# Kernel tuning notes

Measured on AMD Instinct MI355X. Metric: run time of the kernel, lower is better.

## Reference

```python
import jax, jax.numpy as jnp
import numpy as np

LEVEL = 3  # init kwarg: level=3, wavelet_type='db1' (Haar)


def _haar_step(x):
    """One db1/Haar 2x2 stride-2 decomposition on [B,C,H,W].
    conv2d with kernels outer(l,l),outer(l,h),outer(h,l),outer(h,h), l=h=1/sqrt(2),
    reduces to block sum/difference arithmetic with factor 0.5.
    Returns [B, 4*C, H/2, W/2] in the torch code's channel-major layout
    (c0_LL, c0_LH, c0_HL, c0_HH, c1_LL, ...).
    """
    a = x[..., 0::2, 0::2]
    b = x[..., 0::2, 1::2]
    c = x[..., 1::2, 0::2]
    d = x[..., 1::2, 1::2]
    ll = (a + b + c + d) * 0.5
    lh = (a - b + c - d) * 0.5  # low rows x high cols (cross-correlation)
    hl = (a + b - c - d) * 0.5
    hh = (a - b - c + d) * 0.5
    w = jnp.stack([ll, lh, hl, hh], axis=2)  # [B, C, 4, H/2, W/2]
    B, C = x.shape[0], x.shape[1]
    return w.reshape(B, 4 * C, w.shape[3], w.shape[4])


def setup_inputs() -> dict:
    key = jax.random.key(0)
    x = jax.random.normal(key, (4, 32, 512, 512), dtype=jnp.float32)
    return {"x": x}


def reference(x):
    C = x.shape[1]
    current = x
    highs = []
    for _ in range(LEVEL):
        cur4 = _haar_step(current)        # [B, 4C, h, w]
        low = cur4[:, :C]                 # first C of interleaved subband channels (as in torch code)
        highs.append(cur4[:, C:])         # remaining 3C channels
        current = low
    # torch returns (low, [h1, h2, h3, low])
    return (low, highs[0], highs[1], highs[2], low)
```

## Files before the change

kernel.cpp:

```cpp
#include <hip/hip_runtime.h>


__global__ __launch_bounds__(256) void haar_step_kernel(
    const float* __restrict__ in,
    float* __restrict__ low,
    float* __restrict__ high,
    float* __restrict__ low_dup,
    int C, int H, int W, int total)
{
    int tid = blockIdx.x * blockDim.x + threadIdx.x;
    if (tid >= total) return;

    const int OH  = H >> 1;
    const int OW  = W >> 1;
    const int OW2 = OW >> 1;

    int ow2 = tid % OW2;
    int t1  = tid / OW2;
    int oh  = t1 % OH;
    int t2  = t1 / OH;
    int c   = t2 % C;
    int b   = t2 / C;

    const float* rowbase = in + (((size_t)(b * C + c) * H + 2 * oh) * W) + 4 * ow2;
    float4 r0 = *reinterpret_cast<const float4*>(rowbase);
    float4 r1 = *reinterpret_cast<const float4*>(rowbase + W);

    float2 ll, lh, hl, hh;
    ll.x = (r0.x + r0.y + r1.x + r1.y) * 0.5f;
    lh.x = (r0.x - r0.y + r1.x - r1.y) * 0.5f;
    hl.x = (r0.x + r0.y - r1.x - r1.y) * 0.5f;
    hh.x = (r0.x - r0.y - r1.x + r1.y) * 0.5f;
    ll.y = (r0.z + r0.w + r1.z + r1.w) * 0.5f;
    lh.y = (r0.z - r0.w + r1.z - r1.w) * 0.5f;
    hl.y = (r0.z + r0.w - r1.z - r1.w) * 0.5f;
    hh.y = (r0.z - r0.w - r1.z + r1.w) * 0.5f;

    const int    baseoc = 4 * c;
    const size_t cs     = (size_t)OH * OW;
    const size_t sp     = (size_t)oh * OW + 2 * ow2;

    if (baseoc < C) {
        float* p = low + ((size_t)b * C + baseoc) * cs + sp;
        *reinterpret_cast<float2*>(p)          = ll;
        *reinterpret_cast<float2*>(p + cs)     = lh;
        *reinterpret_cast<float2*>(p + 2 * cs) = hl;
        *reinterpret_cast<float2*>(p + 3 * cs) = hh;
        if (low_dup) {
            float* q = low_dup + ((size_t)b * C + baseoc) * cs + sp;
            *reinterpret_cast<float2*>(q)          = ll;
            *reinterpret_cast<float2*>(q + cs)     = lh;
            *reinterpret_cast<float2*>(q + 2 * cs) = hl;
            *reinterpret_cast<float2*>(q + 3 * cs) = hh;
        }
    } else {
        float* p = high + ((size_t)b * (3 * C) + (baseoc - C)) * cs + sp;
        *reinterpret_cast<float2*>(p)          = ll;
        *reinterpret_cast<float2*>(p + cs)     = lh;
        *reinterpret_cast<float2*>(p + 2 * cs) = hl;
        *reinterpret_cast<float2*>(p + 3 * cs) = hh;
    }
}

extern "C" void kernel_launch(void* const* d_in, const int* in_sizes, int n_in,
                              void* d_out, int out_size, void* d_ws, size_t ws_size,
                              hipStream_t stream) {
    const float* x = (const float*)d_in[0];
    float* out = (float*)d_out;

    const int B = 4, C = 32;

    const size_t n_low3  = (size_t)B * C * 64 * 64;
    const size_t n_high1 = (size_t)B * 3 * C * 256 * 256;
    const size_t n_high2 = (size_t)B * 3 * C * 128 * 128;
    const size_t n_high3 = (size_t)B * 3 * C * 64 * 64;

    float* low3_a = out;
    float* high1  = out + n_low3;
    float* high2  = high1 + n_high1;
    float* high3  = high2 + n_high2;
    float* low3_b = high3 + n_high3;

    float* ws1 = (float*)d_ws;
    float* ws2 = ws1 + (size_t)B * C * 256 * 256;

    const int threads = 256;

    {
        int total = B * C * 256 * 128;
        int blocks = (total + threads - 1) / threads;
        haar_step_kernel<<<blocks, threads, 0, stream>>>(
            x, ws1, high1, nullptr, C, 512, 512, total);
    }
    {
        int total = B * C * 128 * 64;
        int blocks = (total + threads - 1) / threads;
        haar_step_kernel<<<blocks, threads, 0, stream>>>(
            ws1, ws2, high2, nullptr, C, 256, 256, total);
    }
    {
        int total = B * C * 64 * 32;
        int blocks = (total + threads - 1) / threads;
        haar_step_kernel<<<blocks, threads, 0, stream>>>(
            ws2, low3_a, high3, low3_b, C, 128, 128, total);
    }
}
```

Before: 246.2 us.

## Fuse three Haar decomposition levels into one register-resident kernel

Replaces three separate Haar-step launches with a single kernel. Each thread loads an 8x8 input patch and computes all three levels in registers, writing each high band directly to its output location. This removes the workspace round trips for the intermediate low bands and two kernel launches. In exchange, register pressure rises, the level-3 stores are scalar and strided across channels, and channels with c>=8 exit early, which leaves work unevenly spread across blocks.

```diff
diff --git a/kernel.cpp b/kernel.cpp
--- a/kernel.cpp
+++ b/kernel.cpp
@@ -1,64 +1,105 @@
 #include <hip/hip_runtime.h>
 
 
-__global__ __launch_bounds__(256) void haar_step_kernel(
-    const float* __restrict__ in,
-    float* __restrict__ low,
-    float* __restrict__ high,
-    float* __restrict__ low_dup,
-    int C, int H, int W, int total)
+#define HAAR(a, b_, c_, d, o0, o1, o2, o3)       \
+    o0 = (a + b_ + c_ + d) * 0.5f;               \
+    o1 = (a - b_ + c_ - d) * 0.5f;               \
+    o2 = (a + b_ - c_ - d) * 0.5f;               \
+    o3 = (a - b_ - c_ + d) * 0.5f;
+
+__global__ __launch_bounds__(256) void haar3_fused(
+    const float* __restrict__ x,
+    float* __restrict__ high1,
+    float* __restrict__ high2,
+    float* __restrict__ high3,
+    float* __restrict__ low3a,
+    float* __restrict__ low3b)
 {
-    int tid = blockIdx.x * blockDim.x + threadIdx.x;
-    if (tid >= total) return;
+    const int tid   = threadIdx.x;
+    const int tx    = tid & 63;
+    const int ty    = tid >> 6;
+    const int tileY = blockIdx.x;
+    const int bc    = blockIdx.y;
+    const int c     = bc & 31;
+    const int b     = bc >> 5;
 
-    const int OH  = H >> 1;
-    const int OW  = W >> 1;
-    const int OW2 = OW >> 1;
+    float w1[4][4][4];
+    {
+        const float* base = x + ((size_t)bc * 512 + (size_t)(tileY * 32 + ty * 8)) * 512
+                              + (size_t)tx * 8;
+        #pragma unroll
+        for (int i = 0; i < 4; ++i) {
+            float4 r0a = *(const float4*)(base + (size_t)(2 * i) * 512);
+            float4 r0b = *(const float4*)(base + (size_t)(2 * i) * 512 + 4);
+            float4 r1a = *(const float4*)(base + (size_t)(2 * i + 1) * 512);
+            float4 r1b = *(const float4*)(base + (size_t)(2 * i + 1) * 512 + 4);
+            HAAR(r0a.x, r0a.y, r1a.x, r1a.y, w1[0][i][0], w1[1][i][0], w1[2][i][0], w1[3][i][0]);
+            HAAR(r0a.z, r0a.w, r1a.z, r1a.w, w1[0][i][1], w1[1][i][1], w1[2][i][1], w1[3][i][1]);
+            HAAR(r0b.x, r0b.y, r1b.x, r1b.y, w1[0][i][2], w1[1][i][2], w1[2][i][2], w1[3][i][2]);
+            HAAR(r0b.z, r0b.w, r1b.z, r1b.w, w1[0][i][3], w1[1][i][3], w1[2][i][3], w1[3][i][3]);
+        }
+    }
 
-    int ow2 = tid % OW2;
-    int t1  = tid / OW2;
-    int oh  = t1 % OH;
-    int t2  = t1 / OH;
-    int c   = t2 % C;
-    int b   = t2 / C;
+    if (c >= 8) {
+        float* hp = high1 + ((size_t)b * 96 + (size_t)(4 * (c - 8))) * (256 * 256)
+                          + (size_t)(tileY * 16 + ty * 4) * 256 + (size_t)tx * 4;
+        #pragma unroll
+        for (int s = 0; s < 4; ++s)
+            #pragma unroll
+            for (int i = 0; i < 4; ++i)
+                *(float4*)(hp + (size_t)s * (256 * 256) + i * 256) =
+                    make_float4(w1[s][i][0], w1[s][i][1], w1[s][i][2], w1[s][i][3]);
+        return;
+    }
 
-    const float* rowbase = in + (((size_t)(b * C + c) * H + 2 * oh) * W) + 4 * ow2;
-    float4 r0 = *reinterpret_cast<const float4*>(rowbase);
-    float4 r1 = *reinterpret_cast<const float4*>(rowbase + W);
+    float w2[16][2][2];
+    #pragma unroll
+    for (int s = 0; s < 4; ++s)
+        #pragma unroll
+        for (int i = 0; i < 2; ++i)
+            #pragma unroll
+            for (int j = 0; j < 2; ++j) {
+                float a  = w1[s][2 * i][2 * j];
+                float bb = w1[s][2 * i][2 * j + 1];
+                float cc = w1[s][2 * i + 1][2 * j];
+                float dd = w1[s][2 * i + 1][2 * j + 1];
+                HAAR(a, bb, cc, dd, w2[4 * s + 0][i][j], w2[4 * s + 1][i][j],
+                                    w2[4 * s + 2][i][j], w2[4 * s + 3][i][j]);
+            }
 
-    float2 ll, lh, hl, hh;
-    ll.x = (r0.x + r0.y + r1.x + r1.y) * 0.5f;
-    lh.x = (r0.x - r0.y + r1.x - r1.y) * 0.5f;
-    hl.x = (r0.x + r0.y - r1.x - r1.y) * 0.5f;
-    hh.x = (r0.x - r0.y - r1.x + r1.y) * 0.5f;
-    ll.y = (r0.z + r0.w + r1.z + r1.w) * 0.5f;
-    lh.y = (r0.z - r0.w + r1.z - r1.w) * 0.5f;
-    hl.y = (r0.z + r0.w - r1.z - r1.w) * 0.5f;
-    hh.y = (r0.z - r0.w - r1.z + r1.w) * 0.5f;
+    if (c >= 2) {
+        float* hp = high2 + ((size_t)b * 96 + (size_t)(16 * (c - 2))) * (128 * 128)
+                          + (size_t)(tileY * 8 + ty * 2) * 128 + (size_t)tx * 2;
+        #pragma unroll
+        for (int j2 = 0; j2 < 16; ++j2)
+            #pragma unroll
+            for (int i = 0; i < 2; ++i)
+                *(float2*)(hp + (size_t)j2 * (128 * 128) + i * 128) =
+                    make_float2(w2[j2][i][0], w2[j2][i][1]);
+        return;
+    }
 
-    const int    baseoc = 4 * c;
-    const size_t cs     = (size_t)OH * OW;
-    const size_t sp     = (size_t)oh * OW + 2 * ow2;
-
-    if (baseoc < C) {
-        float* p = low + ((size_t)b * C + baseoc) * cs + sp;
-        *reinterpret_cast<float2*>(p)          = ll;
-        *reinterpret_cast<float2*>(p + cs)     = lh;
-        *reinterpret_cast<float2*>(p + 2 * cs) = hl;
-        *reinterpret_cast<float2*>(p + 3 * cs) = hh;
-        if (low_dup) {
-            float* q = low_dup + ((size_t)b * C + baseoc) * cs + sp;
-            *reinterpret_cast<float2*>(q)          = ll;
-            *reinterpret_cast<float2*>(q + cs)     = lh;
-            *reinterpret_cast<float2*>(q + 2 * cs) = hl;
-            *reinterpret_cast<float2*>(q + 3 * cs) = hh;
+    const size_t p3  = 64 * 64;
+    const size_t sp3 = (size_t)(tileY * 4 + ty) * 64 + (size_t)tx;
+    #pragma unroll
+    for (int j2 = 0; j2 < 16; ++j2) {
+        float a  = w2[j2][0][0];
+        float bb = w2[j2][0][1];
+        float cc = w2[j2][1][0];
+        float dd = w2[j2][1][1];
+        float v0, v1, v2, v3;
+        HAAR(a, bb, cc, dd, v0, v1, v2, v3);
+        float v[4] = {v0, v1, v2, v3};
+        #pragma unroll
+        for (int s3 = 0; s3 < 4; ++s3) {
+            int ch = 64 * c + 4 * j2 + s3;
+            if (ch < 32) {
+                low3a[((size_t)b * 32 + ch) * p3 + sp3] = v[s3];
+                low3b[((size_t)b * 32 + ch) * p3 + sp3] = v[s3];
+            } else {
+                high3[((size_t)b * 96 + (ch - 32)) * p3 + sp3] = v[s3];
+            }
         }
-    } else {
-        float* p = high + ((size_t)b * (3 * C) + (baseoc - C)) * cs + sp;
-        *reinterpret_cast<float2*>(p)          = ll;
-        *reinterpret_cast<float2*>(p + cs)     = lh;
-        *reinterpret_cast<float2*>(p + 2 * cs) = hl;
-        *reinterpret_cast<float2*>(p + 3 * cs) = hh;
     }
 }
 
@@ -68,40 +109,17 @@
     const float* x = (const float*)d_in[0];
     float* out = (float*)d_out;
 
-    const int B = 4, C = 32;
+    const size_t n_low3  = (size_t)4 * 32 * 64 * 64;
+    const size_t n_high1 = (size_t)4 * 96 * 256 * 256;
+    const size_t n_high2 = (size_t)4 * 96 * 128 * 128;
+    const size_t n_high3 = (size_t)4 * 96 * 64 * 64;
 
-    const size_t n_low3  = (size_t)B * C * 64 * 64;
-    const size_t n_high1 = (size_t)B * 3 * C * 256 * 256;
-    const size_t n_high2 = (size_t)B * 3 * C * 128 * 128;
-    const size_t n_high3 = (size_t)B * 3 * C * 64 * 64;
+    float* low3a = out;
+    float* high1 = out + n_low3;
+    float* high2 = high1 + n_high1;
+    float* high3 = high2 + n_high2;
+    float* low3b = high3 + n_high3;
 
-    float* low3_a = out;
-    float* high1  = out + n_low3;
-    float* high2  = high1 + n_high1;
-    float* high3  = high2 + n_high2;
-    float* low3_b = high3 + n_high3;
-
-    float* ws1 = (float*)d_ws;
-    float* ws2 = ws1 + (size_t)B * C * 256 * 256;
-
-    const int threads = 256;
-
-    {
-        int total = B * C * 256 * 128;
-        int blocks = (total + threads - 1) / threads;
-        haar_step_kernel<<<blocks, threads, 0, stream>>>(
-            x, ws1, high1, nullptr, C, 512, 512, total);
-    }
-    {
-        int total = B * C * 128 * 64;
-        int blocks = (total + threads - 1) / threads;
-        haar_step_kernel<<<blocks, threads, 0, stream>>>(
-            ws1, ws2, high2, nullptr, C, 256, 256, total);
-    }
-    {
-        int total = B * C * 64 * 32;
-        int blocks = (total + threads - 1) / threads;
-        haar_step_kernel<<<blocks, threads, 0, stream>>>(
-            ws2, low3_a, high3, low3_b, C, 128, 128, total);
-    }
+    dim3 grid(16, 128);
+    haar3_fused<<<grid, 256, 0, stream>>>(x, high1, high2, high3, low3a, low3b);
 }
```

Measured after the change: 235.3 us. 1.05x faster.
